# Kernel tuning notes

Measured on AMD Instinct MI355X. Metric: run time of the kernel, lower is better.

Reference implementation:

```python
import jax, jax.numpy as jnp
import numpy as np

N = 50000
E = 800000
D = 128          # in_channels == hidden_channels
L = 3            # num_layers
JK = D * L       # jk 'cat' output
H2 = D // 2      # classifier hidden
C = 2            # out classes
EPS = 1e-5


def setup_inputs() -> dict:
    key = jax.random.key(0)
    ks = jax.random.split(key, 16)
    x = jax.random.normal(ks[0], (N, D), dtype=jnp.float32)
    edge_index = jax.random.randint(ks[1], (2, E), 0, N, dtype=jnp.int64)
    s = 0.05
    Wl = jax.random.normal(ks[2], (L, D, D), dtype=jnp.float32) * s   # lin_l (on aggregated), has bias
    bl = jax.random.normal(ks[3], (L, D), dtype=jnp.float32) * s
    Wr = jax.random.normal(ks[4], (L, D, D), dtype=jnp.float32) * s   # lin_r (on root), no bias
    gamma = jnp.ones((L, D), dtype=jnp.float32)
    beta = jnp.zeros((L, D), dtype=jnp.float32)
    rmean = jax.random.normal(ks[5], (L, D), dtype=jnp.float32) * s
    rvar = jax.random.uniform(ks[6], (L, D), dtype=jnp.float32, minval=0.5, maxval=1.5)
    Wc1 = jax.random.normal(ks[7], (JK, H2), dtype=jnp.float32) * s
    bc1 = jax.random.normal(ks[8], (H2,), dtype=jnp.float32) * s
    Wc2 = jax.random.normal(ks[9], (H2, C), dtype=jnp.float32) * s
    bc2 = jax.random.normal(ks[10], (C,), dtype=jnp.float32) * s
    return {"x": x, "edge_index": edge_index, "Wl": Wl, "bl": bl, "Wr": Wr,
            "gamma": gamma, "beta": beta, "rmean": rmean, "rvar": rvar,
            "Wc1": Wc1, "bc1": bc1, "Wc2": Wc2, "bc2": bc2}


def reference(x, edge_index, Wl, bl, Wr, gamma, beta, rmean, rvar, Wc1, bc1, Wc2, bc2):
    src, dst = edge_index[0], edge_index[1]
    # node in-degree (for mean aggregation), clamp to avoid div-by-zero
    deg = jax.ops.segment_sum(jnp.ones((E,), dtype=x.dtype), dst, num_segments=N)
    inv_deg = 1.0 / jnp.maximum(deg, 1.0)  # [N]

    h = x
    layer_outputs = []
    for i in range(L):
        # SAGEConv(mean): out = lin_l(mean_{j in N(i)} h_j) + lin_r(h_i)
        agg = jax.ops.segment_sum(h[src], dst, num_segments=N) * inv_deg[:, None]  # [N, D]
        h = agg @ Wl[i] + bl[i] + h @ Wr[i]
        # BatchNorm (eval: running stats), then ReLU; Dropout is identity in eval
        h = (h - rmean[i]) * jax.lax.rsqrt(rvar[i] + EPS) * gamma[i] + beta[i]
        h = jax.nn.relu(h)
        layer_outputs.append(h)

    jk = jnp.concatenate(layer_outputs, axis=-1)  # [N, L*D]
    z = jax.nn.relu(jk @ Wc1 + bc1)
    logits = z @ Wc2 + bc2  # [N, 2]
    return logits
```

## Files before the change

### kernel.cpp

```cpp
#include <hip/hip_runtime.h>
#include <hip/hip_fp16.h>
#include <cstdint>
#include <cstddef>

#define DD 128
#define JKD 384
#define EPSV 1e-5f
#define BSH 7
#define NBMAX 512
#define BCAP2 4096
#define PCH 8192
#define PTH 1024
#define BCAP 8192

typedef __attribute__((ext_vector_type(8))) short bf16x8;
typedef __attribute__((ext_vector_type(4))) float f32x4;
#define MFMA(a, b, c) __builtin_amdgcn_mfma_f32_16x16x32_bf16(a, b, c, 0, 0, 0)

__device__ inline unsigned short f2bf_rne(float f) {
  unsigned u = __float_as_uint(f);
  unsigned r = u + 0x7fffu + ((u >> 16) & 1u);
  return (unsigned short)(r >> 16);
}

__device__ inline void split8(const float* s, bf16x8& hi, bf16x8& lo) {
#pragma unroll
  for (int j = 0; j < 8; ++j) {
    float f = s[j];
    unsigned short h = f2bf_rne(f);
    float fh = __uint_as_float((unsigned)h << 16);
    hi[j] = (short)h;
    lo[j] = (short)f2bf_rne(f - fh);
  }
}

__device__ inline void h8_to_f8(uint4 raw, float* out) {
  const __half2* hp = reinterpret_cast<const __half2*>(&raw);
#pragma unroll
  for (int j = 0; j < 4; ++j) {
    float2 f = __half22float2(hp[j]);
    out[2 * j] = f.x;
    out[2 * j + 1] = f.y;
  }
}

__device__ __forceinline__ void gload16(const void* g, void* l) {
  __builtin_amdgcn_global_load_lds(
      (const __attribute__((address_space(1))) unsigned int*)g,
      (__attribute__((address_space(3))) unsigned int*)l, 16, 0, 0);
}

__global__ void init_cursor(int* __restrict__ cursor) {
  int t = threadIdx.x;
  if (t < NBMAX) cursor[t] = t * BCAP2;
}

__global__ __launch_bounds__(PTH) void partition_prep(
    const int* __restrict__ src, const int* __restrict__ dst, int* bucket_cursor,
    unsigned* __restrict__ packed, int E, int nChunks,
    const float* __restrict__ Wl, const float* __restrict__ Wr, bf16x8* __restrict__ wf,
    const float* __restrict__ Wc1, bf16x8* __restrict__ wcf,
    const float* __restrict__ x, unsigned short* __restrict__ x16, int N) {
  __shared__ int h[NBMAX];
  __shared__ int lofs[NBMAX];
  __shared__ int res[NBMAX];
  __shared__ int lcur[NBMAX];
  __shared__ int wsum[4];
  __shared__ int wpref[4];
  __shared__ unsigned stage[PCH];

  if (blockIdx.x < nChunks) {
    int t = threadIdx.x;
    int lane = t & 63;
    int base = blockIdx.x * PCH;
    for (int i = t; i < NBMAX; i += PTH) h[i] = 0;
    __syncthreads();
#pragma unroll
    for (int it = 0; it < PCH / PTH; ++it) {
      int e = base + it * PTH + t;
      if (e < E) {
        int d = __builtin_nontemporal_load(dst + e);
        atomicAdd(&h[d >> BSH], 1);
      }
    }
    __syncthreads();
    int c0 = 0, c1 = 0, s = 0, sc = 0;
    if (t < 256) {
      c0 = h[2 * t];
      c1 = h[2 * t + 1];
      s = c0 + c1;
      sc = s;
#pragma unroll
      for (int off = 1; off < 64; off <<= 1) {
        int u = __shfl_up(sc, off, 64);
        if (lane >= off) sc += u;
      }
      if (lane == 63) wsum[t >> 6] = sc;
    }
    __syncthreads();
    if (t == 0) {
      int a = 0;
#pragma unroll
      for (int w = 0; w < 4; ++w) { wpref[w] = a; a += wsum[w]; }
    }
    __syncthreads();
    if (t < 256) {
      int excl = wpref[t >> 6] + sc - s;
      lofs[2 * t] = excl;
      lofs[2 * t + 1] = excl + c0;
      lcur[2 * t] = excl;
      lcur[2 * t + 1] = excl + c0;
      if (c0 > 0) res[2 * t] = atomicAdd(&bucket_cursor[2 * t], c0);
      if (c1 > 0) res[2 * t + 1] = atomicAdd(&bucket_cursor[2 * t + 1], c1);
    }
    __syncthreads();
#pragma unroll
    for (int it = 0; it < PCH / PTH; ++it) {
      int e = base + it * PTH + t;
      if (e < E) {
        int d = __builtin_nontemporal_load(dst + e);
        int sv = __builtin_nontemporal_load(src + e);
        int pos = atomicAdd(&lcur[d >> BSH], 1);
        stage[pos] = ((unsigned)(d & ((1 << BSH) - 1)) << 16) | (unsigned)(sv & 0xffff);
      }
    }
    __syncthreads();
    int wid = t >> 6;
    for (int b = wid; b < NBMAX; b += PTH / 64) {
      int run = h[b];
      if (run == 0) continue;
      int gbase = res[b], lbase = lofs[b];
      for (int j = lane; j < run; j += 64) packed[gbase + j] = stage[lbase + j];
    }
  } else {
    int sub = threadIdx.x >> 8;
    int t = threadIdx.x & 255;
    int f16blocks = (N * 16 + 255) / 256;
    int vb = (blockIdx.x - nChunks) * 4 + sub;
    if (vb >= 60 + f16blocks) return;
    if (vb < 48) {
      int idx = vb * 256 + t;
      int ln = idx & 63;
      int ksnt = (idx >> 6) & 31;
      int mat = (idx >> 11) & 1;
      int layer = idx >> 12;
      int ks = ksnt >> 3, nt = ksnt & 7;
      int nn = nt * 16 + (ln & 15);
      int k0 = ks * 32 + (ln >> 4) * 8;
      const float* W = (mat ? Wr : Wl) + (size_t)layer * DD * DD;
      float v[8];
#pragma unroll
      for (int j = 0; j < 8; ++j) v[j] = W[(size_t)(k0 + j) * DD + nn];
      bf16x8 hi, lo;
      split8(v, hi, lo);
      size_t base = (size_t)((layer * 2 + mat) * 2) * 2048 + (size_t)ksnt * 64 + ln;
      wf[base] = hi;
      wf[base + 2048] = lo;
    } else if (vb < 60) {
      int idx = (vb - 48) * 256 + t;
      int ln = idx & 63;
      int ksnt = idx >> 6;
      int ks = ksnt >> 2, nt = ksnt & 3;
      int nn = nt * 16 + (ln & 15);
      int k0 = ks * 32 + (ln >> 4) * 8;
      float v[8];
#pragma unroll
      for (int j = 0; j < 8; ++j) v[j] = Wc1[(size_t)(k0 + j) * 64 + nn];
      bf16x8 hi, lo;
      split8(v, hi, lo);
      wcf[idx] = hi;
      wcf[idx + 3072] = lo;
    } else {
      int idx = (vb - 60) * 256 + t;
      int r = idx >> 4, cc = (idx & 15) * 8;
      if (r < N) {
        const float* p = x + (size_t)r * DD + cc;
        float4 a = *reinterpret_cast<const float4*>(p);
        float4 bb = *reinterpret_cast<const float4*>(p + 4);
        __half2 h0 = __floats2half2_rn(a.x, a.y);
        __half2 h1 = __floats2half2_rn(a.z, a.w);
        __half2 h2 = __floats2half2_rn(bb.x, bb.y);
        __half2 h3 = __floats2half2_rn(bb.z, bb.w);
        uint4 o;
        o.x = *reinterpret_cast<unsigned*>(&h0);
        o.y = *reinterpret_cast<unsigned*>(&h1);
        o.z = *reinterpret_cast<unsigned*>(&h2);
        o.w = *reinterpret_cast<unsigned*>(&h3);
        *reinterpret_cast<uint4*>(x16 + (size_t)r * DD + cc) = o;
      }
    }
  }
}

__global__ __launch_bounds__(256) void csr_build(const unsigned* __restrict__ packed,
                                                 const int* __restrict__ bucket_cursor,
                                                 int* __restrict__ row_start,
                                                 int* __restrict__ row_end,
                                                 float* __restrict__ inv_deg,
                                                 unsigned short* __restrict__ col, int N) {
  __shared__ int cntA[128];
  __shared__ int lcur[128];
  __shared__ int wsum2[2];
  __shared__ int wpref2[2];
  __shared__ unsigned short stage[BCAP];
  int t = threadIdx.x;
  int b = blockIdx.x;
  int s0 = b * BCAP2;
  int cnt = bucket_cursor[b] - s0;
  if (t < 128) cntA[t] = 0;
  __syncthreads();
  for (int i = t; i < cnt; i += 256) {
    unsigned p = packed[s0 + i];
    atomicAdd(&cntA[p >> 16], 1);
  }
  __syncthreads();
  if (t < 128) {
    int lane = t & 63, wid = t >> 6;
    int v = cntA[t];
    int sc = v;
#pragma unroll
    for (int off = 1; off < 64; off <<= 1) {
      int u = __shfl_up(sc, off, 64);
      if (lane >= off) sc += u;
    }
    if (lane == 63) wsum2[wid] = sc;
    __syncthreads();
    if (t == 0) { wpref2[0] = 0; wpref2[1] = wsum2[0]; }
    __syncthreads();
    int excl = wpref2[wid] + sc - v;
    lcur[t] = excl;
    int node = b * 128 + t;
    if (node < N) {
      row_start[node] = s0 + excl;
      row_end[node] = s0 + excl + v;
      inv_deg[node] = 1.0f / fmaxf((float)v, 1.0f);
    }
  } else {
    __syncthreads();
    __syncthreads();
  }
  __syncthreads();
  for (int i = t; i < cnt; i += 256) {
    unsigned p = packed[s0 + i];
    int pos = atomicAdd(&lcur[p >> 16], 1);
    unsigned short us = (unsigned short)(p & 0xffff);
    if (pos < BCAP) stage[pos] = us;
    else col[s0 + pos] = us;
  }
  __syncthreads();
  int lim = min(cnt, BCAP);
  for (int i = t; i < lim; i += 256) col[s0 + i] = stage[i];
}

__global__ __launch_bounds__(256) void agg16_kernel(const unsigned short* __restrict__ h16,
                                                    int ldh,
                                                    const int* __restrict__ row_start,
                                                    const int* __restrict__ row_end,
                                                    const unsigned short* __restrict__ col,
                                                    const float* __restrict__ inv_deg,
                                                    unsigned short* __restrict__ agg16, int n) {
  int wib = threadIdx.x >> 6;
  int lane = threadIdx.x & 63;
  int node = blockIdx.x * 4 + wib;
  if (node >= n) return;
  int beg = row_start[node];
  int end = row_end[node];
  int q = lane >> 4, l15 = lane & 15;
  float acc[8];
#pragma unroll
  for (int k = 0; k < 8; ++k) acc[k] = 0.f;

  for (int j0 = beg; j0 < end; j0 += 16) {
    int cnt = end - j0;
    if (cnt > 16) cnt = 16;
    int cidx = (int)col[j0 + min(l15, cnt - 1)];
    uint4 raw[4];
    bool val[4];
#pragma unroll
    for (int k = 0; k < 4; ++k) {
      int e = k * 4 + q;
      int s = __shfl(cidx, e < cnt ? e : 0);
      val[k] = e < cnt;
      if (val[k]) raw[k] = *reinterpret_cast<const uint4*>(h16 + (size_t)s * ldh + l15 * 8);
    }
#pragma unroll
    for (int k = 0; k < 4; ++k) {
      if (val[k]) {
        float f8[8];
        h8_to_f8(raw[k], f8);
#pragma unroll
        for (int c = 0; c < 8; ++c) acc[c] += f8[c];
      }
    }
  }
#pragma unroll
  for (int m = 16; m <= 32; m <<= 1) {
#pragma unroll
    for (int k = 0; k < 8; ++k) acc[k] += __shfl_xor(acc[k], m);
  }
  if (lane < 16) {
    float w = inv_deg[node];
    __half2 h0 = __floats2half2_rn(acc[0] * w, acc[1] * w);
    __half2 h1 = __floats2half2_rn(acc[2] * w, acc[3] * w);
    __half2 h2 = __floats2half2_rn(acc[4] * w, acc[5] * w);
    __half2 h3 = __floats2half2_rn(acc[6] * w, acc[7] * w);
    uint4 o;
    o.x = *reinterpret_cast<unsigned*>(&h0);
    o.y = *reinterpret_cast<unsigned*>(&h1);
    o.z = *reinterpret_cast<unsigned*>(&h2);
    o.w = *reinterpret_cast<unsigned*>(&h3);
    *reinterpret_cast<uint4*>(agg16 + (size_t)node * DD + l15 * 8) = o;
  }
}

__global__ __launch_bounds__(256) void layer_gemm_mfma(
    const unsigned short* __restrict__ hin16, int ldh,
    const unsigned short* __restrict__ agg16,
    const bf16x8* __restrict__ Blh_g, const bf16x8* __restrict__ Bll_g,
    const bf16x8* __restrict__ Brh_g, const bf16x8* __restrict__ Brl_g,
    const float* __restrict__ bl, const float* __restrict__ gamma,
    const float* __restrict__ beta, const float* __restrict__ rmean,
    const float* __restrict__ rvar, unsigned short* __restrict__ out16, int n) {
  __shared__ __align__(16) unsigned char smem[32768];
  int t = threadIdx.x;
  int w = t >> 6, lane = t & 63;
  int lane16 = lane & 15, quad = lane >> 4;
  int row0 = blockIdx.x * 64;
  int m = row0 + w * 16 + lane16;
  bool valid = m < n;
  size_t mrow = (size_t)(valid ? m : 0);
  const unsigned short* ap = agg16 + mrow * DD + quad * 8;
  const unsigned short* hp = hin16 + mrow * (size_t)ldh + quad * 8;

  const bf16x8* halfp = (w == 0) ? Blh_g : (w == 1) ? Bll_g : (w == 2) ? Brh_g : Brl_g;
  unsigned char* sreg = smem + w * 8192;

#pragma unroll
  for (int c = 0; c < 8; ++c) gload16(halfp + c * 64 + lane, sreg + c * 1024);

  bf16x8 Ah[4], Al[4], Hh[4], Hl[4];
#pragma unroll
  for (int ks = 0; ks < 4; ++ks) {
    float a8[8], h8[8];
    if (valid) {
      uint4 ra = *reinterpret_cast<const uint4*>(ap + ks * 32);
      uint4 rh = *reinterpret_cast<const uint4*>(hp + ks * 32);
      h8_to_f8(ra, a8);
      h8_to_f8(rh, h8);
    } else {
#pragma unroll
      for (int j = 0; j < 8; ++j) { a8[j] = 0.f; h8[j] = 0.f; }
    }
    split8(a8, Ah[ks], Al[ks]);
    split8(h8, Hh[ks], Hl[ks]);
  }

  f32x4 acc[8];
#pragma unroll
  for (int nt = 0; nt < 8; ++nt) acc[nt] = (f32x4){0.f, 0.f, 0.f, 0.f};

  const bf16x8* sB = reinterpret_cast<const bf16x8*>(smem);
  __syncthreads();

#pragma unroll
  for (int ks = 0; ks < 4; ++ks) {
    bf16x8 B0[8], B1[8];
#pragma unroll
    for (int nt = 0; nt < 8; ++nt) B0[nt] = sB[nt * 64 + lane];
#pragma unroll
    for (int nt = 0; nt < 8; ++nt) acc[nt] = MFMA(Ah[ks], B0[nt], acc[nt]);
#pragma unroll
    for (int nt = 0; nt < 8; ++nt) B1[nt] = sB[512 + nt * 64 + lane];
#pragma unroll
    for (int nt = 0; nt < 8; ++nt) acc[nt] = MFMA(Al[ks], B0[nt], acc[nt]);
#pragma unroll
    for (int nt = 0; nt < 8; ++nt) acc[nt] = MFMA(Ah[ks], B1[nt], acc[nt]);
#pragma unroll
    for (int nt = 0; nt < 8; ++nt) B0[nt] = sB[1024 + nt * 64 + lane];
#pragma unroll
    for (int nt = 0; nt < 8; ++nt) acc[nt] = MFMA(Hh[ks], B0[nt], acc[nt]);
#pragma unroll
    for (int nt = 0; nt < 8; ++nt) B1[nt] = sB[1536 + nt * 64 + lane];
#pragma unroll
    for (int nt = 0; nt < 8; ++nt) acc[nt] = MFMA(Hl[ks], B0[nt], acc[nt]);
#pragma unroll
    for (int nt = 0; nt < 8; ++nt) acc[nt] = MFMA(Hh[ks], B1[nt], acc[nt]);
    if (ks < 3) {
      __syncthreads();
#pragma unroll
      for (int c = 0; c < 8; ++c)
        gload16(halfp + (ks + 1) * 512 + c * 64 + lane, sreg + c * 1024);
      __syncthreads();
    }
  }

#pragma unroll
  for (int nt = 0; nt < 8; ++nt) {
    int c = nt * 16 + lane16;
    float sc = gamma[c] * rsqrtf(rvar[c] + EPSV);
    float sh = (bl[c] - rmean[c]) * sc + beta[c];
#pragma unroll
    for (int r = 0; r < 4; ++r) {
      int orow = row0 + w * 16 + quad * 4 + r;
      if (orow < n) {
        float v = fmaxf(fmaf(acc[nt][r], sc, sh), 0.f);
        __half hv = __float2half_rn(v);
        out16[(size_t)orow * JKD + c] = *reinterpret_cast<unsigned short*>(&hv);
      }
    }
  }
}

__global__ __launch_bounds__(256) void gemm2_cls(
    const unsigned short* __restrict__ gsrc, int ldg,
    const unsigned short* __restrict__ agg16,
    const bf16x8* __restrict__ Blh_g, const bf16x8* __restrict__ Bll_g,
    const bf16x8* __restrict__ Brh_g, const bf16x8* __restrict__ Brl_g,
    const float* __restrict__ bl, const float* __restrict__ gamma,
    const float* __restrict__ beta, const float* __restrict__ rmean,
    const float* __restrict__ rvar,
    const unsigned short* __restrict__ jk16, const bf16x8* __restrict__ wcf,
    const float* __restrict__ bc1, const float* __restrict__ Wc2,
    const float* __restrict__ bc2, float* __restrict__ out, int n) {
  __shared__ __align__(16) unsigned char smem[17408 + 24576];
  unsigned short (*sOut)[16][136] = reinterpret_cast<unsigned short(*)[16][136]>(smem);
  float (*sZ)[65] = reinterpret_cast<float(*)[65]>(smem);
  unsigned char* clsw = smem + 17408;
  const bf16x8* sB = reinterpret_cast<const bf16x8*>(smem);
  const bf16x8* csB = reinterpret_cast<const bf16x8*>(clsw);
  int t = threadIdx.x;
  int w = t >> 6, lane = t & 63;
  int lane16 = lane & 15, quad = lane >> 4;
  int row0 = blockIdx.x * 64;
  int m = row0 + w * 16 + lane16;
  bool valid = m < n;
  size_t mrow = (size_t)(valid ? m : 0);
  const unsigned short* ap = agg16 + mrow * DD + quad * 8;
  const unsigned short* hp = gsrc + mrow * (size_t)ldg + quad * 8;

  const bf16x8* halfp = (w == 0) ? Blh_g : (w == 1) ? Bll_g : (w == 2) ? Brh_g : Brl_g;
  unsigned char* sreg = smem + w * 8192;

#pragma unroll
  for (int c = 0; c < 8; ++c) gload16(halfp + c * 64 + lane, sreg + c * 1024);

  bf16x8 Ah[4], Al[4], Hh[4], Hl[4];
#pragma unroll
  for (int ks = 0; ks < 4; ++ks) {
    float a8[8], h8[8];
    if (valid) {
      uint4 ra = *reinterpret_cast<const uint4*>(ap + ks * 32);
      uint4 rh = *reinterpret_cast<const uint4*>(hp + ks * 32);
      h8_to_f8(ra, a8);
      h8_to_f8(rh, h8);
    } else {
#pragma unroll
      for (int j = 0; j < 8; ++j) { a8[j] = 0.f; h8[j] = 0.f; }
    }
    split8(a8, Ah[ks], Al[ks]);
    split8(h8, Hh[ks], Hl[ks]);
  }

  f32x4 acc[8];
#pragma unroll
  for (int nt = 0; nt < 8; ++nt) acc[nt] = (f32x4){0.f, 0.f, 0.f, 0.f};

  __syncthreads();

#pragma unroll
  for (int ks = 0; ks < 4; ++ks) {
    bf16x8 B0[8], B1[8];
#pragma unroll
    for (int nt = 0; nt < 8; ++nt) B0[nt] = sB[nt * 64 + lane];
#pragma unroll
    for (int nt = 0; nt < 8; ++nt) acc[nt] = MFMA(Ah[ks], B0[nt], acc[nt]);
#pragma unroll
    for (int nt = 0; nt < 8; ++nt) B1[nt] = sB[512 + nt * 64 + lane];
#pragma unroll
    for (int nt = 0; nt < 8; ++nt) acc[nt] = MFMA(Al[ks], B0[nt], acc[nt]);
#pragma unroll
    for (int nt = 0; nt < 8; ++nt) acc[nt] = MFMA(Ah[ks], B1[nt], acc[nt]);
#pragma unroll
    for (int nt = 0; nt < 8; ++nt) B0[nt] = sB[1024 + nt * 64 + lane];
#pragma unroll
    for (int nt = 0; nt < 8; ++nt) acc[nt] = MFMA(Hh[ks], B0[nt], acc[nt]);
#pragma unroll
    for (int nt = 0; nt < 8; ++nt) B1[nt] = sB[1536 + nt * 64 + lane];
#pragma unroll
    for (int nt = 0; nt < 8; ++nt) acc[nt] = MFMA(Hl[ks], B0[nt], acc[nt]);
#pragma unroll
    for (int nt = 0; nt < 8; ++nt) acc[nt] = MFMA(Hh[ks], B1[nt], acc[nt]);
    if (ks < 3) {
      __syncthreads();
#pragma unroll
      for (int c = 0; c < 8; ++c)
        gload16(halfp + (ks + 1) * 512 + c * 64 + lane, sreg + c * 1024);
      __syncthreads();
    }
  }
  __syncthreads();

#pragma unroll
  for (int nt = 0; nt < 8; ++nt) {
    int c = nt * 16 + lane16;
    float sc = gamma[c] * rsqrtf(rvar[c] + EPSV);
    float sh = (bl[c] - rmean[c]) * sc + beta[c];
#pragma unroll
    for (int r = 0; r < 4; ++r) {
      float v = fmaxf(fmaf(acc[nt][r], sc, sh), 0.f);
      __half hv = __float2half_rn(v);
      sOut[w][quad * 4 + r][c] = *reinterpret_cast<unsigned short*>(&hv);
    }
  }

  const unsigned short* jp = jk16 + mrow * JKD + quad * 8;
  f32x4 cacc[4];
#pragma unroll
  for (int nt = 0; nt < 4; ++nt) cacc[nt] = (f32x4){0.f, 0.f, 0.f, 0.f};

#pragma unroll
  for (int g = 0; g < 4; ++g) {
    __syncthreads();
#pragma unroll
    for (int c = 0; c < 6; ++c) {
      int ch = w * 6 + c;
      const bf16x8* gp = (ch < 12) ? (wcf + g * 768 + ch * 64)
                                   : (wcf + 3072 + g * 768 + (ch - 12) * 64);
      gload16(gp + lane, clsw + ch * 1024);
    }
    __syncthreads();
#pragma unroll
    for (int k3 = 0; k3 < 3; ++k3) {
      int ks = g * 3 + k3;
      float a8[8];
      if (ks < 8) {
        if (valid) {
          uint4 raw = *reinterpret_cast<const uint4*>(jp + ks * 32);
          h8_to_f8(raw, a8);
        } else {
#pragma unroll
          for (int j = 0; j < 8; ++j) a8[j] = 0.f;
        }
      } else {
        uint4 raw = *reinterpret_cast<const uint4*>(&sOut[w][lane16][(ks - 8) * 32 + quad * 8]);
        h8_to_f8(raw, a8);
      }
      bf16x8 Jh, Jl;
      split8(a8, Jh, Jl);
      bf16x8 B0[4], B1[4];
#pragma unroll
      for (int nt = 0; nt < 4; ++nt) B0[nt] = csB[k3 * 256 + nt * 64 + lane];
#pragma unroll
      for (int nt = 0; nt < 4; ++nt) cacc[nt] = MFMA(Jh, B0[nt], cacc[nt]);
#pragma unroll
      for (int nt = 0; nt < 4; ++nt) B1[nt] = csB[768 + k3 * 256 + nt * 64 + lane];
#pragma unroll
      for (int nt = 0; nt < 4; ++nt) cacc[nt] = MFMA(Jl, B0[nt], cacc[nt]);
#pragma unroll
      for (int nt = 0; nt < 4; ++nt) cacc[nt] = MFMA(Jh, B1[nt], cacc[nt]);
    }
  }
  __syncthreads();

#pragma unroll
  for (int nt = 0; nt < 4; ++nt) {
    int c = nt * 16 + lane16;
    float b1 = bc1[c];
#pragma unroll
    for (int r = 0; r < 4; ++r)
      sZ[w * 16 + quad * 4 + r][c] = fmaxf(cacc[nt][r] + b1, 0.f);
  }
  __syncthreads();

  if (t < 128) {
    int r = t >> 1, j = t & 1;
    int gr = row0 + r;
    if (gr < n) {
      float s = bc2[j];
#pragma unroll
      for (int c = 0; c < 64; ++c) s = fmaf(sZ[r][c], Wc2[c * 2 + j], s);
      out[(size_t)gr * 2 + j] = s;
    }
  }
}


extern "C" void kernel_launch(void* const* d_in, const int* in_sizes, int n_in,
                              void* d_out, int out_size, void* d_ws, size_t ws_size,
                              hipStream_t stream) {
  const float* x = (const float*)d_in[0];
  const int* ei = (const int*)d_in[1];
  const float* Wl = (const float*)d_in[2];
  const float* bl = (const float*)d_in[3];
  const float* Wr = (const float*)d_in[4];
  const float* gamma = (const float*)d_in[5];
  const float* beta = (const float*)d_in[6];
  const float* rmean = (const float*)d_in[7];
  const float* rvar = (const float*)d_in[8];
  const float* Wc1 = (const float*)d_in[9];
  const float* bc1 = (const float*)d_in[10];
  const float* Wc2 = (const float*)d_in[11];
  const float* bc2 = (const float*)d_in[12];
  float* out = (float*)d_out;

  const int N = in_sizes[0] / DD;
  const int E = in_sizes[1] / 2;
  const int* src = ei;
  const int* dst = ei + E;

  auto align = [](size_t v) { return (v + 255) & ~(size_t)255; };
  char* ws = (char*)d_ws;
  size_t off = 0;
  int* row_start = (int*)(ws + off);  off = align(off + sizeof(int) * (size_t)N);
  int* row_end = (int*)(ws + off);    off = align(off + sizeof(int) * (size_t)N);
  unsigned short* col = (unsigned short*)(ws + off); off = align(off + sizeof(short) * (size_t)NBMAX * BCAP2);
  float* inv_deg = (float*)(ws + off); off = align(off + sizeof(float) * (size_t)N);
  unsigned* packed = (unsigned*)(ws + off); off = align(off + sizeof(unsigned) * (size_t)NBMAX * BCAP2);
  int* bucket_cursor = (int*)(ws + off); off = align(off + sizeof(int) * NBMAX);
  unsigned short* x16 = (unsigned short*)(ws + off);   off = align(off + sizeof(short) * (size_t)N * DD);
  unsigned short* agg16 = (unsigned short*)(ws + off); off = align(off + sizeof(short) * (size_t)N * DD);
  unsigned short* jk16 = (unsigned short*)(ws + off);  off = align(off + sizeof(short) * (size_t)N * JKD);
  bf16x8* wf = (bf16x8*)(ws + off);  off = align(off + (size_t)16 * 3 * 2 * 2 * 2048);
  bf16x8* wcf = (bf16x8*)(ws + off); off = align(off + (size_t)16 * 2 * 3072);

  const int nbuck = (N + 127) >> BSH;
  const int nChunks = (E + PCH - 1) / PCH;
  int f16blocks = (N * 16 + 255) / 256;
  int prepBlocks = (60 + f16blocks + 3) / 4;

  init_cursor<<<1, NBMAX, 0, stream>>>(bucket_cursor);
  partition_prep<<<nChunks + prepBlocks, PTH, 0, stream>>>(
      src, dst, bucket_cursor, packed, E, nChunks, Wl, Wr, wf, Wc1, wcf, x, x16, N);
  csr_build<<<nbuck, 256, 0, stream>>>(packed, bucket_cursor, row_start, row_end, inv_deg, col, N);

  int nTiles = (N + 63) / 64;
  for (int i = 0; i < 3; ++i) {
    const unsigned short* gsrc = (i == 0) ? x16 : (jk16 + (size_t)(i - 1) * DD);
    int ldg = (i == 0) ? DD : JKD;
    agg16_kernel<<<(N + 3) / 4, 256, 0, stream>>>(gsrc, ldg, row_start, row_end, col, inv_deg, agg16, N);
    bf16x8* Wlf = wf + (size_t)(i * 2 + 0) * 2 * 2048;
    bf16x8* Wrf = wf + (size_t)(i * 2 + 1) * 2 * 2048;
    if (i < 2) {
      layer_gemm_mfma<<<nTiles, 256, 0, stream>>>(
          gsrc, ldg, agg16, Wlf, Wlf + 2048, Wrf, Wrf + 2048,
          bl + (size_t)i * DD, gamma + (size_t)i * DD, beta + (size_t)i * DD,
          rmean + (size_t)i * DD, rvar + (size_t)i * DD, jk16 + (size_t)i * DD, N);
    } else {
      gemm2_cls<<<nTiles, 256, 0, stream>>>(
          gsrc, ldg, agg16, Wlf, Wlf + 2048, Wrf, Wrf + 2048,
          bl + (size_t)i * DD, gamma + (size_t)i * DD, beta + (size_t)i * DD,
          rmean + (size_t)i * DD, rvar + (size_t)i * DD,
          jk16, wcf, bc1, Wc2, bc2, out, N);
    }
  }
}
```

Measured before the change: 284.3 us.

## Fuse neighbor mean-aggregation into per-layer GEMM kernels via shared-memory staging

Removes the standalone aggregation kernel. Each 64-row GEMM tile now gathers and averages its own nodes' neighbor features into an XOR-swizzled LDS buffer, then feeds them to the MFMA stage, for both the middle layers and the final layer-plus-classifier kernel. This drops the global agg16 round trip and one launch per layer. In exchange, each wave walks 16 nodes serially instead of one node per wave across many blocks, and LDS use per block grows, which can lower occupancy and the number of gathers in flight. In the classifier kernel the aggregation buffer shares space with the classifier-weight region, so correctness depends on when those weights are loaded.

```diff
diff --git a/kernel.cpp b/kernel.cpp
--- a/kernel.cpp
+++ b/kernel.cpp
@@ -252,76 +252,79 @@
   for (int i = t; i < lim; i += 256) col[s0 + i] = stage[i];
 }
 
-__global__ __launch_bounds__(256) void agg16_kernel(const unsigned short* __restrict__ h16,
-                                                    int ldh,
-                                                    const int* __restrict__ row_start,
-                                                    const int* __restrict__ row_end,
-                                                    const unsigned short* __restrict__ col,
-                                                    const float* __restrict__ inv_deg,
-                                                    unsigned short* __restrict__ agg16, int n) {
-  int wib = threadIdx.x >> 6;
-  int lane = threadIdx.x & 63;
-  int node = blockIdx.x * 4 + wib;
-  if (node >= n) return;
-  int beg = row_start[node];
-  int end = row_end[node];
+
+__device__ __forceinline__ void agg_phase(
+    const unsigned short* __restrict__ hin16, int ldh,
+    const int* __restrict__ row_start, const int* __restrict__ row_end,
+    const unsigned short* __restrict__ col, const float* __restrict__ inv_deg,
+    unsigned char* sagg, int row0, int w, int lane, int n) {
   int q = lane >> 4, l15 = lane & 15;
-  float acc[8];
-#pragma unroll
-  for (int k = 0; k < 8; ++k) acc[k] = 0.f;
-
-  for (int j0 = beg; j0 < end; j0 += 16) {
-    int cnt = end - j0;
-    if (cnt > 16) cnt = 16;
-    int cidx = (int)col[j0 + min(l15, cnt - 1)];
-    uint4 raw[4];
-    bool val[4];
-#pragma unroll
-    for (int k = 0; k < 4; ++k) {
-      int e = k * 4 + q;
-      int s = __shfl(cidx, e < cnt ? e : 0);
-      val[k] = e < cnt;
-      if (val[k]) raw[k] = *reinterpret_cast<const uint4*>(h16 + (size_t)s * ldh + l15 * 8);
-    }
-#pragma unroll
-    for (int k = 0; k < 4; ++k) {
-      if (val[k]) {
-        float f8[8];
-        h8_to_f8(raw[k], f8);
-#pragma unroll
-        for (int c = 0; c < 8; ++c) acc[c] += f8[c];
-      }
-    }
-  }
-#pragma unroll
-  for (int m = 16; m <= 32; m <<= 1) {
-#pragma unroll
-    for (int k = 0; k < 8; ++k) acc[k] += __shfl_xor(acc[k], m);
-  }
-  if (lane < 16) {
-    float w = inv_deg[node];
-    __half2 h0 = __floats2half2_rn(acc[0] * w, acc[1] * w);
-    __half2 h1 = __floats2half2_rn(acc[2] * w, acc[3] * w);
-    __half2 h2 = __floats2half2_rn(acc[4] * w, acc[5] * w);
-    __half2 h3 = __floats2half2_rn(acc[6] * w, acc[7] * w);
-    uint4 o;
-    o.x = *reinterpret_cast<unsigned*>(&h0);
-    o.y = *reinterpret_cast<unsigned*>(&h1);
-    o.z = *reinterpret_cast<unsigned*>(&h2);
-    o.w = *reinterpret_cast<unsigned*>(&h3);
-    *reinterpret_cast<uint4*>(agg16 + (size_t)node * DD + l15 * 8) = o;
-  }
-}
-
-__global__ __launch_bounds__(256) void layer_gemm_mfma(
+#pragma unroll 1
+  for (int i = 0; i < 16; ++i) {
+    int node = row0 + w * 16 + i;
+    float acc[8];
+#pragma unroll
+    for (int k = 0; k < 8; ++k) acc[k] = 0.f;
+    if (node < n) {
+      int beg = row_start[node];
+      int end = row_end[node];
+      for (int j0 = beg; j0 < end; j0 += 16) {
+        int cnt = end - j0;
+        if (cnt > 16) cnt = 16;
+        int cidx = (int)col[j0 + min(l15, cnt - 1)];
+        uint4 raw[4];
+        bool val[4];
+#pragma unroll
+        for (int k = 0; k < 4; ++k) {
+          int e = k * 4 + q;
+          int s = __shfl(cidx, e < cnt ? e : 0);
+          val[k] = e < cnt;
+          if (val[k]) raw[k] = *reinterpret_cast<const uint4*>(hin16 + (size_t)s * ldh + l15 * 8);
+        }
+#pragma unroll
+        for (int k = 0; k < 4; ++k) {
+          if (val[k]) {
+            float f8[8];
+            h8_to_f8(raw[k], f8);
+#pragma unroll
+            for (int c = 0; c < 8; ++c) acc[c] += f8[c];
+          }
+        }
+      }
+#pragma unroll
+      for (int mm = 16; mm <= 32; mm <<= 1) {
+#pragma unroll
+        for (int k = 0; k < 8; ++k) acc[k] += __shfl_xor(acc[k], mm);
+      }
+    }
+    if (lane < 16) {
+      uint4 o = {0u, 0u, 0u, 0u};
+      if (node < n) {
+        float wg = inv_deg[node];
+        __half2 h0 = __floats2half2_rn(acc[0] * wg, acc[1] * wg);
+        __half2 h1 = __floats2half2_rn(acc[2] * wg, acc[3] * wg);
+        __half2 h2 = __floats2half2_rn(acc[4] * wg, acc[5] * wg);
+        __half2 h3 = __floats2half2_rn(acc[6] * wg, acc[7] * wg);
+        o.x = *reinterpret_cast<unsigned*>(&h0);
+        o.y = *reinterpret_cast<unsigned*>(&h1);
+        o.z = *reinterpret_cast<unsigned*>(&h2);
+        o.w = *reinterpret_cast<unsigned*>(&h3);
+      }
+      *reinterpret_cast<uint4*>(sagg + (w * 16 + i) * 256 + ((l15 ^ i) << 4)) = o;
+    }
+  }
+}
+
+__global__ __launch_bounds__(256) void layer_fused(
     const unsigned short* __restrict__ hin16, int ldh,
-    const unsigned short* __restrict__ agg16,
+    const int* __restrict__ row_start, const int* __restrict__ row_end,
+    const unsigned short* __restrict__ col, const float* __restrict__ inv_deg,
     const bf16x8* __restrict__ Blh_g, const bf16x8* __restrict__ Bll_g,
     const bf16x8* __restrict__ Brh_g, const bf16x8* __restrict__ Brl_g,
     const float* __restrict__ bl, const float* __restrict__ gamma,
     const float* __restrict__ beta, const float* __restrict__ rmean,
     const float* __restrict__ rvar, unsigned short* __restrict__ out16, int n) {
-  __shared__ __align__(16) unsigned char smem[32768];
+  __shared__ __align__(16) unsigned char smem[32768 + 16384];
   int t = threadIdx.x;
   int w = t >> 6, lane = t & 63;
   int lane16 = lane & 15, quad = lane >> 4;
@@ -329,28 +332,34 @@
   int m = row0 + w * 16 + lane16;
   bool valid = m < n;
   size_t mrow = (size_t)(valid ? m : 0);
-  const unsigned short* ap = agg16 + mrow * DD + quad * 8;
   const unsigned short* hp = hin16 + mrow * (size_t)ldh + quad * 8;
 
   const bf16x8* halfp = (w == 0) ? Blh_g : (w == 1) ? Bll_g : (w == 2) ? Brh_g : Brl_g;
   unsigned char* sreg = smem + w * 8192;
+  unsigned char* sagg = smem + 32768;
 
 #pragma unroll
   for (int c = 0; c < 8; ++c) gload16(halfp + c * 64 + lane, sreg + c * 1024);
+
+  uint4 rh4[4];
+#pragma unroll
+  for (int ks = 0; ks < 4; ++ks) {
+    if (valid) rh4[ks] = *reinterpret_cast<const uint4*>(hp + ks * 32);
+    else rh4[ks] = (uint4){0u, 0u, 0u, 0u};
+  }
+
+  agg_phase(hin16, ldh, row_start, row_end, col, inv_deg, sagg, row0, w, lane, n);
+
+  __syncthreads();
 
   bf16x8 Ah[4], Al[4], Hh[4], Hl[4];
 #pragma unroll
   for (int ks = 0; ks < 4; ++ks) {
     float a8[8], h8[8];
-    if (valid) {
-      uint4 ra = *reinterpret_cast<const uint4*>(ap + ks * 32);
-      uint4 rh = *reinterpret_cast<const uint4*>(hp + ks * 32);
-      h8_to_f8(ra, a8);
-      h8_to_f8(rh, h8);
-    } else {
-#pragma unroll
-      for (int j = 0; j < 8; ++j) { a8[j] = 0.f; h8[j] = 0.f; }
-    }
+    uint4 ra = *reinterpret_cast<const uint4*>(
+        sagg + (w * 16 + lane16) * 256 + (((ks * 4 + quad) ^ lane16) << 4));
+    h8_to_f8(ra, a8);
+    h8_to_f8(rh4[ks], h8);
     split8(a8, Ah[ks], Al[ks]);
     split8(h8, Hh[ks], Hl[ks]);
   }
@@ -360,7 +369,6 @@
   for (int nt = 0; nt < 8; ++nt) acc[nt] = (f32x4){0.f, 0.f, 0.f, 0.f};
 
   const bf16x8* sB = reinterpret_cast<const bf16x8*>(smem);
-  __syncthreads();
 
 #pragma unroll
   for (int ks = 0; ks < 4; ++ks) {
@@ -413,7 +421,8 @@
 
 __global__ __launch_bounds__(256) void gemm2_cls(
     const unsigned short* __restrict__ gsrc, int ldg,
-    const unsigned short* __restrict__ agg16,
+    const int* __restrict__ row_start, const int* __restrict__ row_end,
+    const unsigned short* __restrict__ col, const float* __restrict__ inv_deg,
     const bf16x8* __restrict__ Blh_g, const bf16x8* __restrict__ Bll_g,
     const bf16x8* __restrict__ Brh_g, const bf16x8* __restrict__ Brl_g,
     const float* __restrict__ bl, const float* __restrict__ gamma,
@@ -422,10 +431,11 @@
     const unsigned short* __restrict__ jk16, const bf16x8* __restrict__ wcf,
     const float* __restrict__ bc1, const float* __restrict__ Wc2,
     const float* __restrict__ bc2, float* __restrict__ out, int n) {
-  __shared__ __align__(16) unsigned char smem[17408 + 24576];
+  __shared__ __align__(16) unsigned char smem[32768 + 24576];
   unsigned short (*sOut)[16][136] = reinterpret_cast<unsigned short(*)[16][136]>(smem);
   float (*sZ)[65] = reinterpret_cast<float(*)[65]>(smem);
-  unsigned char* clsw = smem + 17408;
+  unsigned char* clsw = smem + 32768;
+  unsigned char* sagg = smem + 32768;
   const bf16x8* sB = reinterpret_cast<const bf16x8*>(smem);
   const bf16x8* csB = reinterpret_cast<const bf16x8*>(clsw);
   int t = threadIdx.x;
@@ -435,7 +445,6 @@
   int m = row0 + w * 16 + lane16;
   bool valid = m < n;
   size_t mrow = (size_t)(valid ? m : 0);
-  const unsigned short* ap = agg16 + mrow * DD + quad * 8;
   const unsigned short* hp = gsrc + mrow * (size_t)ldg + quad * 8;
 
   const bf16x8* halfp = (w == 0) ? Blh_g : (w == 1) ? Bll_g : (w == 2) ? Brh_g : Brl_g;
@@ -444,19 +453,25 @@
 #pragma unroll
   for (int c = 0; c < 8; ++c) gload16(halfp + c * 64 + lane, sreg + c * 1024);
 
+  uint4 rh4[4];
+#pragma unroll
+  for (int ks = 0; ks < 4; ++ks) {
+    if (valid) rh4[ks] = *reinterpret_cast<const uint4*>(hp + ks * 32);
+    else rh4[ks] = (uint4){0u, 0u, 0u, 0u};
+  }
+
+  agg_phase(gsrc, ldg, row_start, row_end, col, inv_deg, sagg, row0, w, lane, n);
+
+  __syncthreads();
+
   bf16x8 Ah[4], Al[4], Hh[4], Hl[4];
 #pragma unroll
   for (int ks = 0; ks < 4; ++ks) {
     float a8[8], h8[8];
-    if (valid) {
-      uint4 ra = *reinterpret_cast<const uint4*>(ap + ks * 32);
-      uint4 rh = *reinterpret_cast<const uint4*>(hp + ks * 32);
-      h8_to_f8(ra, a8);
-      h8_to_f8(rh, h8);
-    } else {
-#pragma unroll
-      for (int j = 0; j < 8; ++j) { a8[j] = 0.f; h8[j] = 0.f; }
-    }
+    uint4 ra = *reinterpret_cast<const uint4*>(
+        sagg + (w * 16 + lane16) * 256 + (((ks * 4 + quad) ^ lane16) << 4));
+    h8_to_f8(ra, a8);
+    h8_to_f8(rh4[ks], h8);
     split8(a8, Ah[ks], Al[ks]);
     split8(h8, Hh[ks], Hl[ks]);
   }
@@ -464,8 +479,6 @@
   f32x4 acc[8];
 #pragma unroll
   for (int nt = 0; nt < 8; ++nt) acc[nt] = (f32x4){0.f, 0.f, 0.f, 0.f};
-
-  __syncthreads();
 
 #pragma unroll
   for (int ks = 0; ks < 4; ++ks) {
@@ -618,7 +631,6 @@
   unsigned* packed = (unsigned*)(ws + off); off = align(off + sizeof(unsigned) * (size_t)NBMAX * BCAP2);
   int* bucket_cursor = (int*)(ws + off); off = align(off + sizeof(int) * NBMAX);
   unsigned short* x16 = (unsigned short*)(ws + off);   off = align(off + sizeof(short) * (size_t)N * DD);
-  unsigned short* agg16 = (unsigned short*)(ws + off); off = align(off + sizeof(short) * (size_t)N * DD);
   unsigned short* jk16 = (unsigned short*)(ws + off);  off = align(off + sizeof(short) * (size_t)N * JKD);
   bf16x8* wf = (bf16x8*)(ws + off);  off = align(off + (size_t)16 * 3 * 2 * 2 * 2048);
   bf16x8* wcf = (bf16x8*)(ws + off); off = align(off + (size_t)16 * 2 * 3072);
@@ -637,17 +649,18 @@
   for (int i = 0; i < 3; ++i) {
     const unsigned short* gsrc = (i == 0) ? x16 : (jk16 + (size_t)(i - 1) * DD);
     int ldg = (i == 0) ? DD : JKD;
-    agg16_kernel<<<(N + 3) / 4, 256, 0, stream>>>(gsrc, ldg, row_start, row_end, col, inv_deg, agg16, N);
     bf16x8* Wlf = wf + (size_t)(i * 2 + 0) * 2 * 2048;
     bf16x8* Wrf = wf + (size_t)(i * 2 + 1) * 2 * 2048;
     if (i < 2) {
-      layer_gemm_mfma<<<nTiles, 256, 0, stream>>>(
-          gsrc, ldg, agg16, Wlf, Wlf + 2048, Wrf, Wrf + 2048,
+      layer_fused<<<nTiles, 256, 0, stream>>>(
+          gsrc, ldg, row_start, row_end, col, inv_deg,
+          Wlf, Wlf + 2048, Wrf, Wrf + 2048,
           bl + (size_t)i * DD, gamma + (size_t)i * DD, beta + (size_t)i * DD,
           rmean + (size_t)i * DD, rvar + (size_t)i * DD, jk16 + (size_t)i * DD, N);
     } else {
       gemm2_cls<<<nTiles, 256, 0, stream>>>(
-          gsrc, ldg, agg16, Wlf, Wlf + 2048, Wrf, Wrf + 2048,
+          gsrc, ldg, row_start, row_end, col, inv_deg,
+          Wlf, Wlf + 2048, Wrf, Wrf + 2048,
           bl + (size_t)i * DD, gamma + (size_t)i * DD, beta + (size_t)i * DD,
           rmean + (size_t)i * DD, rvar + (size_t)i * DD,
           jk16, wcf, bc1, Wc2, bc2, out, N);
```

Measured after the change: 387.0 us. 36.1% more time.
